# Kernel tuning notes

Hardware: AMD Instinct MI355X
Metric: run time of the kernel (lower is better)

Reference implementation:

```python
import jax, jax.numpy as jnp
import numpy as np

B, M, SV, OV, R, L, V, E = 256, 10, 32, 32, 128, 12, 1000, 64
M2 = M * M
STATE_DIM = (SV + 1) * M2  # 3300
OBJ_DIM = OV * M2          # 3200


def setup_inputs() -> dict:
    key = jax.random.key(0)
    ks = jax.random.split(key, 24)
    s = 0.02
    inp = {
        "state": jax.random.randint(ks[0], (B, M2), 0, SV),
        "obj": jax.random.randint(ks[1], (B, M2), 0, OV),
        "text": jax.random.randint(ks[2], (B, L), 0, V),
        # state MLP [STATE_DIM,128,128,R]
        "Ws1": jax.random.normal(ks[3], (STATE_DIM, 128)) * s,
        "bs1": jnp.zeros((128,)),
        "Ws2": jax.random.normal(ks[4], (128, 128)) * s,
        "bs2": jnp.zeros((128,)),
        "Ws3": jax.random.normal(ks[5], (128, R)) * s,
        "bs3": jnp.zeros((R,)),
        # object MLP [OBJ_DIM,128,128,R]
        "Wo1": jax.random.normal(ks[6], (OBJ_DIM, 128)) * s,
        "bo1": jnp.zeros((128,)),
        "Wo2": jax.random.normal(ks[7], (128, 128)) * s,
        "bo2": jnp.zeros((128,)),
        "Wo3": jax.random.normal(ks[8], (128, R)) * s,
        "bo3": jnp.zeros((R,)),
        # LSTM text encoder: embedding + single-layer LSTM with hidden=R
        "emb": jax.random.normal(ks[9], (V, E)) * s,
        "Wih": jax.random.normal(ks[10], (E, 4 * R)) * s,
        "Whh": jax.random.normal(ks[11], (R, 4 * R)) * s,
        "b_lstm": jnp.zeros((4 * R,)),
    }
    return inp


def _mlp(x, W1, b1, W2, b2, W3, b3):
    h = jax.nn.relu(x @ W1 + b1)
    h = jax.nn.relu(h @ W2 + b2)
    return h @ W3 + b3


def _lstm_last_hidden(text, emb, Wih, Whh, b):
    # text: (B, L) ids -> final hidden (B, R)
    x = emb[text]                      # (B, L, E)
    xs = jnp.swapaxes(x, 0, 1)         # (L, B, E)
    h0 = jnp.zeros((text.shape[0], R), x.dtype)
    c0 = jnp.zeros((text.shape[0], R), x.dtype)

    def step(carry, xt):
        h, c = carry
        g = xt @ Wih + h @ Whh + b     # (B, 4R)
        i, f, gg, o = jnp.split(g, 4, axis=-1)
        c = jax.nn.sigmoid(f) * c + jax.nn.sigmoid(i) * jnp.tanh(gg)
        h = jax.nn.sigmoid(o) * jnp.tanh(c)
        return (h, c), None

    (h, _), _ = jax.lax.scan(step, (h0, c0), xs)
    return h


def reference(state, obj, text, Ws1, bs1, Ws2, bs2, Ws3, bs3,
              Wo1, bo1, Wo2, bo2, Wo3, bo3, emb, Wih, Whh, b_lstm):
    b = state.shape[0]
    # one-hot encodings (torch scatter_ over channel dim)
    state_oh = jax.nn.one_hot(state, SV, dtype=jnp.float32)   # (B, 100, SV)
    obj_oh = jax.nn.one_hot(obj, OV, dtype=jnp.float32)       # (B, 100, OV)

    # repeat each map map_dim^2 times; copy p gets a one-hot of agent position p
    pos = jnp.eye(M2, dtype=jnp.float32)[None, :, :, None]    # (1, 100 copies, 100 cells, 1)
    state_rep = jnp.broadcast_to(state_oh[:, None], (b, M2, M2, SV))
    state_inp = jnp.concatenate(
        [state_rep, jnp.broadcast_to(pos, (b, M2, M2, 1))], axis=-1
    ).reshape(b * M2, STATE_DIM)
    obj_inp = jnp.broadcast_to(obj_oh[:, None], (b, M2, M2, OV)).reshape(b * M2, OBJ_DIM)

    state_out = _mlp(state_inp, Ws1, bs1, Ws2, bs2, Ws3, bs3)   # (B*100, R)
    object_out = _mlp(obj_inp, Wo1, bo1, Wo2, bo2, Wo3, bo3)    # (B*100, R)

    # text is identical across the 100 copies -> encode once, broadcast
    h = _lstm_last_hidden(text, emb, Wih, Whh, b_lstm)          # (B, R)
    lstm_out = jnp.broadcast_to(h[:, None], (b, M2, R)).reshape(b * M2, R)

    values = state_out * object_out * lstm_out                 # (B*100, R)
    map_pred = values.sum(1).reshape(b, M, M)
    return map_pred
```

## Files before the change

### kernel.cpp

```cpp
#include <hip/hip_runtime.h>


#define B_   256
#define M2_  100
#define R_   128
#define L_   12
#define E_   64
#define NT   1024

typedef _Float16 half2v __attribute__((ext_vector_type(2)));
typedef _Float16 f16x8  __attribute__((ext_vector_type(8)));
typedef float    f32x4  __attribute__((ext_vector_type(4)));

__device__ __forceinline__ float sigf(float x) { return 1.f / (1.f + expf(-x)); }

__device__ __forceinline__ uint pk16(float a, float b) {
    half2v h; h.x = (_Float16)a; h.y = (_Float16)b;
    return __builtin_bit_cast(uint, h);
}

__device__ __forceinline__ float fdot2u(uint a, uint b, float c) {
    half2v ha = __builtin_bit_cast(half2v, a);
    half2v hb = __builtin_bit_cast(half2v, b);
#if __has_builtin(__builtin_amdgcn_fdot2)
    return __builtin_amdgcn_fdot2(ha, hb, c, false);
#else
    return c + (float)ha.x * (float)hb.x + (float)ha.y * (float)hb.y;
#endif
}

#define X6(OP) OP(0) OP(1) OP(2) OP(3) OP(4) OP(5)

__global__ __launch_bounds__(NT, 4) void uvfa_kernel(
    const int* __restrict__ state, const int* __restrict__ obj, const int* __restrict__ text,
    const float* __restrict__ Ws1, const float* __restrict__ bs1,
    const float* __restrict__ Ws2, const float* __restrict__ bs2,
    const float* __restrict__ Ws3, const float* __restrict__ bs3,
    const float* __restrict__ Wo1, const float* __restrict__ bo1,
    const float* __restrict__ Wo2, const float* __restrict__ bo2,
    const float* __restrict__ Wo3, const float* __restrict__ bo3,
    const float* __restrict__ emb, const float* __restrict__ Wih,
    const float* __restrict__ Whh, const float* __restrict__ b_lstm,
    float* __restrict__ out)
{
    const int b   = blockIdx.x;
    const int tid = threadIdx.x;

    __shared__ __align__(16) uint  U[14848];
    __shared__ __align__(16) float part[NT];
    __shared__ __align__(16) float hbuf[R_];
    __shared__ __align__(16) uint  hpair[R_ / 2];
    __shared__ __align__(16) float tmp[R_], tmp2[R_], wbuf[R_], ubuf[R_], bsbuf[R_];
    __shared__ int   idx_o[M2_], idx_s[M2_], tids[L_];
    __shared__ float c0s;

    float* xw   = (float*)U;
    float* xemb = (float*)(U + 6144);

    const int lane = tid & 63;
    const int wv   = tid >> 6;
    const int m16  = lane & 15;
    const int kg   = lane >> 4;

    f16x8 af[2][4];
    #pragma unroll
    for (int tt = 0; tt < 2; ++tt) {
        int col = (2 * wv + tt) * 16 + m16;
        #pragma unroll
        for (int s = 0; s < 4; ++s) {
            int kb = s * 32 + kg * 8;
            #pragma unroll
            for (int e = 0; e < 8; ++e)
                af[tt][s][e] = (_Float16)Whh[(kb + e) * 512 + col];
        }
    }

    if (tid < M2_) idx_o[tid] = obj[b * M2_ + tid];
    else if (tid >= 128 && tid < 128 + M2_) idx_s[tid - 128] = state[b * M2_ + tid - 128];
    else if (tid >= 256 && tid < 256 + L_) tids[tid - 256] = text[b * L_ + tid - 256];
    else if (tid >= 384 && tid < 448) hpair[tid - 384] = 0u;
    __syncthreads();
    if (tid < L_ * E_) xemb[tid] = emb[tids[tid >> 6] * E_ + (tid & 63)];
    __syncthreads();

    {
        const int col = tid & 511, th = tid >> 9;
        float bl = b_lstm[col];
        #define DA(i) float a##i = bl;
        X6(DA)
        const float* xe = xemb + (th * 6) * E_;
        #pragma unroll 8
        for (int e = 0; e < E_; ++e) {
            float we = Wih[e * 512 + col];
            #define FA(i) a##i = fmaf(xe[(i) * E_ + e], we, a##i);
            X6(FA)
        }
        #define SA(i) xw[(th * 6 + (i)) * 512 + col] = a##i;
        X6(SA)
    }
    __syncthreads();

    float cst = 0.f;
    for (int t = 0; t < L_; ++t) {
        f16x8 bf[4];
        #pragma unroll
        for (int s = 0; s < 4; ++s) {
            uint4 hb = *(const uint4*)&hpair[s * 16 + kg * 4];
            bf[s] = __builtin_bit_cast(f16x8, hb);
        }
        #pragma unroll
        for (int tt = 0; tt < 2; ++tt) {
            int colb = (2 * wv + tt) * 16 + kg * 4;
            f32x4 acc = *(const f32x4*)&xw[t * 512 + colb];
            #pragma unroll
            for (int s = 0; s < 4; ++s)
                acc = __builtin_amdgcn_mfma_f32_16x16x32_f16(af[tt][s], bf[s], acc, 0, 0, 0);
            if (m16 == 0) {
                part[colb + 0] = acc[0];
                part[colb + 1] = acc[1];
                part[colb + 2] = acc[2];
                part[colb + 3] = acc[3];
            }
        }
        __syncthreads();
        if (tid < R_) {
            float gi = part[tid], gf = part[R_ + tid], gg = part[2 * R_ + tid], go = part[3 * R_ + tid];
            cst = sigf(gf) * cst + sigf(gi) * tanhf(gg);
            float hn = sigf(go) * tanhf(cst);
            hbuf[tid] = hn;
            float hs = __shfl_down(hn, 1, 64);
            if (!(tid & 1)) hpair[tid >> 1] = pk16(hn, hs);
        }
        __syncthreads();
    }

    #pragma unroll
    for (int idx = tid; idx < 64 * 128; idx += NT) {
        int jp = idx >> 7, kk = idx & 127;
        U[idx] = pk16(Ws2[(2 * jp) * R_ + kk], Ws2[(2 * jp + 1) * R_ + kk]);
    }

    const int k = tid & 127, qq = tid >> 7;
    {
        float acc = 0.f;
        int c0i = qq * 13, c1i = c0i + 13 < M2_ ? c0i + 13 : M2_;
        for (int c = c0i; c < c1i; ++c)
            acc += Wo1[(c * 32 + idx_o[c]) * R_ + k];
        part[qq * R_ + k] = acc;
    }
    __syncthreads();
    if (tid < R_) {
        float a = bo1[tid];
        #pragma unroll
        for (int q8 = 0; q8 < 8; ++q8) a += part[q8 * R_ + tid];
        tmp[tid] = fmaxf(a, 0.f);
    }
    __syncthreads();
    {
        float s0 = 0.f, s1 = 0.f, s2 = 0.f, s3 = 0.f;
        int j0 = qq * 16;
        #pragma unroll
        for (int j = 0; j < 16; j += 4) {
            s0 = fmaf(tmp[j0 + j + 0], Wo2[(j0 + j + 0) * R_ + k], s0);
            s1 = fmaf(tmp[j0 + j + 1], Wo2[(j0 + j + 1) * R_ + k], s1);
            s2 = fmaf(tmp[j0 + j + 2], Wo2[(j0 + j + 2) * R_ + k], s2);
            s3 = fmaf(tmp[j0 + j + 3], Wo2[(j0 + j + 3) * R_ + k], s3);
        }
        part[qq * R_ + k] = (s0 + s1) + (s2 + s3);
    }
    __syncthreads();
    if (tid < R_) {
        float a = bo2[tid];
        #pragma unroll
        for (int q8 = 0; q8 < 8; ++q8) a += part[q8 * R_ + tid];
        tmp2[tid] = fmaxf(a, 0.f);
    }
    __syncthreads();
    {
        float s0 = 0.f, s1 = 0.f, s2 = 0.f, s3 = 0.f;
        int j0 = qq * 16;
        #pragma unroll
        for (int j = 0; j < 16; j += 4) {
            s0 = fmaf(tmp2[j0 + j + 0], Wo3[(j0 + j + 0) * R_ + k], s0);
            s1 = fmaf(tmp2[j0 + j + 1], Wo3[(j0 + j + 1) * R_ + k], s1);
            s2 = fmaf(tmp2[j0 + j + 2], Wo3[(j0 + j + 2) * R_ + k], s2);
            s3 = fmaf(tmp2[j0 + j + 3], Wo3[(j0 + j + 3) * R_ + k], s3);
        }
        part[qq * R_ + k] = (s0 + s1) + (s2 + s3);
    }
    __syncthreads();
    if (tid < R_) {
        float a = bo3[tid];
        #pragma unroll
        for (int q8 = 0; q8 < 8; ++q8) a += part[q8 * R_ + tid];
        wbuf[tid] = a * hbuf[tid];
    }
    __syncthreads();

    {
        float s0 = 0.f, s1 = 0.f, s2 = 0.f, s3 = 0.f;
        int j0 = qq * 16;
        const float4* w3 = reinterpret_cast<const float4*>(&Ws3[k * R_ + j0]);
        #pragma unroll
        for (int jj = 0; jj < 4; ++jj) {
            float4 v = w3[jj];
            s0 = fmaf(v.x, wbuf[j0 + jj * 4 + 0], s0);
            s1 = fmaf(v.y, wbuf[j0 + jj * 4 + 1], s1);
            s2 = fmaf(v.z, wbuf[j0 + jj * 4 + 2], s2);
            s3 = fmaf(v.w, wbuf[j0 + jj * 4 + 3], s3);
        }
        part[qq * R_ + k] = (s0 + s1) + (s2 + s3);
    }
    if (tid >= 960) {
        int j = tid - 960;
        float s = bs3[j] * wbuf[j] + bs3[j + 64] * wbuf[j + 64];
        s += __shfl_down(s, 32, 64);
        s += __shfl_down(s, 16, 64);
        s += __shfl_down(s, 8, 64);
        s += __shfl_down(s, 4, 64);
        s += __shfl_down(s, 2, 64);
        s += __shfl_down(s, 1, 64);
        if (j == 0) c0s = s;
    }
    __syncthreads();
    if (tid < R_) {
        float a = 0.f;
        #pragma unroll
        for (int q8 = 0; q8 < 8; ++q8) a += part[q8 * R_ + tid];
        ubuf[tid] = a;
    }
    __syncthreads();

    {
        float acc = 0.f;
        int c0i = qq * 13, c1i = c0i + 13 < M2_ ? c0i + 13 : M2_;
        for (int c = c0i; c < c1i; ++c)
            acc += Ws1[(c * 33 + idx_s[c]) * R_ + k];
        part[qq * R_ + k] = acc;
    }
    __syncthreads();
    if (tid < R_) {
        float a = bs1[tid];
        #pragma unroll
        for (int q8 = 0; q8 < 8; ++q8) a += part[q8 * R_ + tid];
        bsbuf[tid] = a;
    }
    __syncthreads();

    #pragma unroll 4
    for (int pass = 0; pass < 13; ++pass) {
        int idx = pass * NT + tid;
        if (idx < M2_ * R_) {
            int j = idx & 127, p = idx >> 7;
            float v = fmaxf(bsbuf[j] + Ws1[(p * 33 + 32) * R_ + j], 0.f);
            float v2 = __shfl_down(v, 1, 64);
            if (!(j & 1)) U[8192 + (j >> 1) * 104 + p] = pk16(v, v2);
        }
    }
    __syncthreads();

    if (tid < 400) {
        const int pq = tid >> 4, ko = tid & 15;
        const uint* Wsp = U + 8 * ko;
        const uint* Hp  = U + 8192 + 4 * pq;
        float4 uA = *(const float4*)&ubuf[8 * ko];
        float4 uB = *(const float4*)&ubuf[8 * ko + 4];
        float4 bA = *(const float4*)&bs2[8 * ko];
        float4 bB = *(const float4*)&bs2[8 * ko + 4];
        float acc[4][8];
        #pragma unroll
        for (int pi = 0; pi < 4; ++pi)
            #pragma unroll
            for (int r = 0; r < 8; ++r) acc[pi][r] = 0.f;
        #pragma unroll 2
        for (int jp = 0; jp < 64; ++jp) {
            uint4 hq = *(const uint4*)(Hp  + jp * 104);
            uint4 w0 = *(const uint4*)(Wsp + jp * 128);
            uint4 w1 = *(const uint4*)(Wsp + jp * 128 + 4);
            #pragma unroll
            for (int pi = 0; pi < 4; ++pi) {
                uint hh = pi == 0 ? hq.x : pi == 1 ? hq.y : pi == 2 ? hq.z : hq.w;
                acc[pi][0] = fdot2u(hh, w0.x, acc[pi][0]);
                acc[pi][1] = fdot2u(hh, w0.y, acc[pi][1]);
                acc[pi][2] = fdot2u(hh, w0.z, acc[pi][2]);
                acc[pi][3] = fdot2u(hh, w0.w, acc[pi][3]);
                acc[pi][4] = fdot2u(hh, w1.x, acc[pi][4]);
                acc[pi][5] = fdot2u(hh, w1.y, acc[pi][5]);
                acc[pi][6] = fdot2u(hh, w1.z, acc[pi][6]);
                acc[pi][7] = fdot2u(hh, w1.w, acc[pi][7]);
            }
        }
        #pragma unroll
        for (int pi = 0; pi < 4; ++pi) {
            float s = fmaxf(acc[pi][0] + bA.x, 0.f) * uA.x + fmaxf(acc[pi][1] + bA.y, 0.f) * uA.y
                    + fmaxf(acc[pi][2] + bA.z, 0.f) * uA.z + fmaxf(acc[pi][3] + bA.w, 0.f) * uA.w
                    + fmaxf(acc[pi][4] + bB.x, 0.f) * uB.x + fmaxf(acc[pi][5] + bB.y, 0.f) * uB.y
                    + fmaxf(acc[pi][6] + bB.z, 0.f) * uB.z + fmaxf(acc[pi][7] + bB.w, 0.f) * uB.w;
            s += __shfl_xor(s, 1, 64);
            s += __shfl_xor(s, 2, 64);
            s += __shfl_xor(s, 4, 64);
            s += __shfl_xor(s, 8, 64);
            if (ko == 0) out[b * M2_ + 4 * pq + pi] = s + c0s;
        }
    }
}

extern "C" void kernel_launch(void* const* d_in, const int* in_sizes, int n_in,
                              void* d_out, int out_size, void* d_ws, size_t ws_size,
                              hipStream_t stream) {
    const int*   state  = (const int*)d_in[0];
    const int*   obj    = (const int*)d_in[1];
    const int*   text   = (const int*)d_in[2];
    const float* Ws1    = (const float*)d_in[3];
    const float* bs1    = (const float*)d_in[4];
    const float* Ws2    = (const float*)d_in[5];
    const float* bs2    = (const float*)d_in[6];
    const float* Ws3    = (const float*)d_in[7];
    const float* bs3    = (const float*)d_in[8];
    const float* Wo1    = (const float*)d_in[9];
    const float* bo1    = (const float*)d_in[10];
    const float* Wo2    = (const float*)d_in[11];
    const float* bo2    = (const float*)d_in[12];
    const float* Wo3    = (const float*)d_in[13];
    const float* bo3    = (const float*)d_in[14];
    const float* emb    = (const float*)d_in[15];
    const float* Wih    = (const float*)d_in[16];
    const float* Whh    = (const float*)d_in[17];
    const float* b_lstm = (const float*)d_in[18];
    float* out = (float*)d_out;

    hipLaunchKernelGGL(uvfa_kernel, dim3(B_), dim3(NT), 0, stream,
                       state, obj, text, Ws1, bs1, Ws2, bs2, Ws3, bs3,
                       Wo1, bo1, Wo2, bo2, Wo3, bo3, emb, Wih, Whh, b_lstm, out);
}
```

Baseline: 46.76 us.

## Move LSTM input projection and state-MLP layer-2 onto MFMA matrix instructions

Replaces the scalar FMA input projection (xemb @ Wih) with 16x16x32 f16 MFMA tiles, zero-padding the 12 timesteps to 16. Replaces the fdot2-based per-position layer-2 GEMM with MFMA tiles over 14 waves, using padded shared-memory layouts (stride 66 and 132) to limit bank conflicts. The relu and dot-with-u epilogue is then reduced across two N-halves through a new shared buffer. This adds fp16 rounding to the input projection, extra LDS footprint and one more barrier.

Result: faster. 39.34 us (-15.9%).

```diff
diff --git a/kernel.cpp b/kernel.cpp
--- a/kernel.cpp
+++ b/kernel.cpp
@@ -18,18 +18,6 @@
     half2v h; h.x = (_Float16)a; h.y = (_Float16)b;
     return __builtin_bit_cast(uint, h);
 }
-
-__device__ __forceinline__ float fdot2u(uint a, uint b, float c) {
-    half2v ha = __builtin_bit_cast(half2v, a);
-    half2v hb = __builtin_bit_cast(half2v, b);
-#if __has_builtin(__builtin_amdgcn_fdot2)
-    return __builtin_amdgcn_fdot2(ha, hb, c, false);
-#else
-    return c + (float)ha.x * (float)hb.x + (float)ha.y * (float)hb.y;
-#endif
-}
-
-#define X6(OP) OP(0) OP(1) OP(2) OP(3) OP(4) OP(5)
 
 __global__ __launch_bounds__(NT, 4) void uvfa_kernel(
     const int* __restrict__ state, const int* __restrict__ obj, const int* __restrict__ text,
@@ -46,21 +34,22 @@
     const int b   = blockIdx.x;
     const int tid = threadIdx.x;
 
-    __shared__ __align__(16) uint  U[14848];
+    __shared__ __align__(16) uint  U[15840];
     __shared__ __align__(16) float part[NT];
     __shared__ __align__(16) float hbuf[R_];
     __shared__ __align__(16) uint  hpair[R_ / 2];
     __shared__ __align__(16) float tmp[R_], tmp2[R_], wbuf[R_], ubuf[R_], bsbuf[R_];
+    __shared__ float redw2[2][112];
     __shared__ int   idx_o[M2_], idx_s[M2_], tids[L_];
     __shared__ float c0s;
 
     float* xw   = (float*)U;
-    float* xemb = (float*)(U + 6144);
+    float* xemb = (float*)(U + 8192);
 
     const int lane = tid & 63;
     const int wv   = tid >> 6;
     const int m16  = lane & 15;
-    const int kg   = lane >> 4;
+    const int kgrp = lane >> 4;
 
     f16x8 af[2][4];
     #pragma unroll
@@ -68,7 +57,7 @@
         int col = (2 * wv + tt) * 16 + m16;
         #pragma unroll
         for (int s = 0; s < 4; ++s) {
-            int kb = s * 32 + kg * 8;
+            int kb = s * 32 + kgrp * 8;
             #pragma unroll
             for (int e = 0; e < 8; ++e)
                 af[tt][s][e] = (_Float16)Whh[(kb + e) * 512 + col];
@@ -80,23 +69,37 @@
     else if (tid >= 256 && tid < 256 + L_) tids[tid - 256] = text[b * L_ + tid - 256];
     else if (tid >= 384 && tid < 448) hpair[tid - 384] = 0u;
     __syncthreads();
-    if (tid < L_ * E_) xemb[tid] = emb[tids[tid >> 6] * E_ + (tid & 63)];
-    __syncthreads();
-
-    {
-        const int col = tid & 511, th = tid >> 9;
-        float bl = b_lstm[col];
-        #define DA(i) float a##i = bl;
-        X6(DA)
-        const float* xe = xemb + (th * 6) * E_;
-        #pragma unroll 8
-        for (int e = 0; e < E_; ++e) {
-            float we = Wih[e * 512 + col];
-            #define FA(i) a##i = fmaf(xe[(i) * E_ + e], we, a##i);
-            X6(FA)
-        }
-        #define SA(i) xw[(th * 6 + (i)) * 512 + col] = a##i;
-        X6(SA)
+    if (tid < L_ * E_) xemb[(tid >> 6) * 66 + (tid & 63)] = emb[tids[tid >> 6] * E_ + (tid & 63)];
+    else if (tid < L_ * E_ + 264) ((float*)(U + 8192 + 792))[tid - L_ * E_] = 0.f;
+    __syncthreads();
+
+    {
+        f16x8 ax[2];
+        #pragma unroll
+        for (int s = 0; s < 2; ++s) {
+            #pragma unroll
+            for (int e = 0; e < 8; ++e)
+                ax[s][e] = (_Float16)xemb[m16 * 66 + s * 32 + kgrp * 8 + e];
+        }
+        #pragma unroll
+        for (int h = 0; h < 2; ++h) {
+            int col = (wv * 2 + h) * 16 + m16;
+            float bl = b_lstm[col];
+            f32x4 acc = { bl, bl, bl, bl };
+            #pragma unroll
+            for (int s = 0; s < 2; ++s) {
+                f16x8 bx;
+                #pragma unroll
+                for (int e = 0; e < 8; ++e)
+                    bx[e] = (_Float16)Wih[(s * 32 + kgrp * 8 + e) * 512 + col];
+                acc = __builtin_amdgcn_mfma_f32_16x16x32_f16(ax[s], bx, acc, 0, 0, 0);
+            }
+            if (kgrp < 3) {
+                #pragma unroll
+                for (int r = 0; r < 4; ++r)
+                    xw[(kgrp * 4 + r) * 512 + col] = acc[r];
+            }
+        }
     }
     __syncthreads();
 
@@ -105,12 +108,12 @@
         f16x8 bf[4];
         #pragma unroll
         for (int s = 0; s < 4; ++s) {
-            uint4 hb = *(const uint4*)&hpair[s * 16 + kg * 4];
+            uint4 hb = *(const uint4*)&hpair[s * 16 + kgrp * 4];
             bf[s] = __builtin_bit_cast(f16x8, hb);
         }
         #pragma unroll
         for (int tt = 0; tt < 2; ++tt) {
-            int colb = (2 * wv + tt) * 16 + kg * 4;
+            int colb = (2 * wv + tt) * 16 + kgrp * 4;
             f32x4 acc = *(const f32x4*)&xw[t * 512 + colb];
             #pragma unroll
             for (int s = 0; s < 4; ++s)
@@ -137,7 +140,7 @@
     #pragma unroll
     for (int idx = tid; idx < 64 * 128; idx += NT) {
         int jp = idx >> 7, kk = idx & 127;
-        U[idx] = pk16(Ws2[(2 * jp) * R_ + kk], Ws2[(2 * jp + 1) * R_ + kk]);
+        U[jp * 132 + kk] = pk16(Ws2[(2 * jp) * R_ + kk], Ws2[(2 * jp + 1) * R_ + kk]);
     }
 
     const int k = tid & 127, qq = tid >> 7;
@@ -254,55 +257,64 @@
             int j = idx & 127, p = idx >> 7;
             float v = fmaxf(bsbuf[j] + Ws1[(p * 33 + 32) * R_ + j], 0.f);
             float v2 = __shfl_down(v, 1, 64);
-            if (!(j & 1)) U[8192 + (j >> 1) * 104 + p] = pk16(v, v2);
-        }
-    }
-    __syncthreads();
-
-    if (tid < 400) {
-        const int pq = tid >> 4, ko = tid & 15;
-        const uint* Wsp = U + 8 * ko;
-        const uint* Hp  = U + 8192 + 4 * pq;
-        float4 uA = *(const float4*)&ubuf[8 * ko];
-        float4 uB = *(const float4*)&ubuf[8 * ko + 4];
-        float4 bA = *(const float4*)&bs2[8 * ko];
-        float4 bB = *(const float4*)&bs2[8 * ko + 4];
-        float acc[4][8];
-        #pragma unroll
-        for (int pi = 0; pi < 4; ++pi)
-            #pragma unroll
-            for (int r = 0; r < 8; ++r) acc[pi][r] = 0.f;
-        #pragma unroll 2
-        for (int jp = 0; jp < 64; ++jp) {
-            uint4 hq = *(const uint4*)(Hp  + jp * 104);
-            uint4 w0 = *(const uint4*)(Wsp + jp * 128);
-            uint4 w1 = *(const uint4*)(Wsp + jp * 128 + 4);
-            #pragma unroll
-            for (int pi = 0; pi < 4; ++pi) {
-                uint hh = pi == 0 ? hq.x : pi == 1 ? hq.y : pi == 2 ? hq.z : hq.w;
-                acc[pi][0] = fdot2u(hh, w0.x, acc[pi][0]);
-                acc[pi][1] = fdot2u(hh, w0.y, acc[pi][1]);
-                acc[pi][2] = fdot2u(hh, w0.z, acc[pi][2]);
-                acc[pi][3] = fdot2u(hh, w0.w, acc[pi][3]);
-                acc[pi][4] = fdot2u(hh, w1.x, acc[pi][4]);
-                acc[pi][5] = fdot2u(hh, w1.y, acc[pi][5]);
-                acc[pi][6] = fdot2u(hh, w1.z, acc[pi][6]);
-                acc[pi][7] = fdot2u(hh, w1.w, acc[pi][7]);
+            if (!(j & 1)) U[8448 + p * 66 + (j >> 1)] = pk16(v, v2);
+        }
+    }
+    if (tid < 792) U[8448 + 6600 + tid] = 0u;
+    __syncthreads();
+
+    if (wv < 14) {
+        const int mtile = wv >> 1, nhalf = wv & 1;
+        const uint* Ap = U + 8448 + (mtile * 16 + m16) * 66;
+        f16x8 A[4];
+        #pragma unroll
+        for (int s = 0; s < 4; ++s) {
+            int jb = s * 16 + kgrp * 4;
+            uint4 av = { Ap[jb + 0], Ap[jb + 1], Ap[jb + 2], Ap[jb + 3] };
+            A[s] = __builtin_bit_cast(f16x8, av);
+        }
+        f32x4 acc[4] = { {0,0,0,0}, {0,0,0,0}, {0,0,0,0}, {0,0,0,0} };
+        #pragma unroll
+        for (int nt = 0; nt < 4; ++nt) {
+            int ko = (nhalf * 4 + nt) * 16 + m16;
+            #pragma unroll
+            for (int s = 0; s < 4; ++s) {
+                const uint* Bp = U + (s * 16 + kgrp * 4) * 132 + ko;
+                uint4 bv = { Bp[0], Bp[132], Bp[264], Bp[396] };
+                acc[nt] = __builtin_amdgcn_mfma_f32_16x16x32_f16(
+                    A[s], __builtin_bit_cast(f16x8, bv), acc[nt], 0, 0, 0);
             }
         }
-        #pragma unroll
-        for (int pi = 0; pi < 4; ++pi) {
-            float s = fmaxf(acc[pi][0] + bA.x, 0.f) * uA.x + fmaxf(acc[pi][1] + bA.y, 0.f) * uA.y
-                    + fmaxf(acc[pi][2] + bA.z, 0.f) * uA.z + fmaxf(acc[pi][3] + bA.w, 0.f) * uA.w
-                    + fmaxf(acc[pi][4] + bB.x, 0.f) * uB.x + fmaxf(acc[pi][5] + bB.y, 0.f) * uB.y
-                    + fmaxf(acc[pi][6] + bB.z, 0.f) * uB.z + fmaxf(acc[pi][7] + bB.w, 0.f) * uB.w;
-            s += __shfl_xor(s, 1, 64);
-            s += __shfl_xor(s, 2, 64);
-            s += __shfl_xor(s, 4, 64);
-            s += __shfl_xor(s, 8, 64);
-            if (ko == 0) out[b * M2_ + 4 * pq + pi] = s + c0s;
-        }
-    }
+        float vs0 = 0.f, vs1 = 0.f, vs2 = 0.f, vs3 = 0.f;
+        #pragma unroll
+        for (int nt = 0; nt < 4; ++nt) {
+            int ko = (nhalf * 4 + nt) * 16 + m16;
+            float bb = bs2[ko], uu = ubuf[ko];
+            vs0 = fmaf(fmaxf(acc[nt][0] + bb, 0.f), uu, vs0);
+            vs1 = fmaf(fmaxf(acc[nt][1] + bb, 0.f), uu, vs1);
+            vs2 = fmaf(fmaxf(acc[nt][2] + bb, 0.f), uu, vs2);
+            vs3 = fmaf(fmaxf(acc[nt][3] + bb, 0.f), uu, vs3);
+        }
+        vs0 += __shfl_xor(vs0, 1, 64); vs0 += __shfl_xor(vs0, 2, 64);
+        vs0 += __shfl_xor(vs0, 4, 64); vs0 += __shfl_xor(vs0, 8, 64);
+        vs1 += __shfl_xor(vs1, 1, 64); vs1 += __shfl_xor(vs1, 2, 64);
+        vs1 += __shfl_xor(vs1, 4, 64); vs1 += __shfl_xor(vs1, 8, 64);
+        vs2 += __shfl_xor(vs2, 1, 64); vs2 += __shfl_xor(vs2, 2, 64);
+        vs2 += __shfl_xor(vs2, 4, 64); vs2 += __shfl_xor(vs2, 8, 64);
+        vs3 += __shfl_xor(vs3, 1, 64); vs3 += __shfl_xor(vs3, 2, 64);
+        vs3 += __shfl_xor(vs3, 4, 64); vs3 += __shfl_xor(vs3, 8, 64);
+        if (m16 == 0) {
+            int pr = mtile * 16 + kgrp * 4;
+            redw2[nhalf][pr + 0] = vs0;
+            redw2[nhalf][pr + 1] = vs1;
+            redw2[nhalf][pr + 2] = vs2;
+            redw2[nhalf][pr + 3] = vs3;
+        }
+    }
+    __syncthreads();
+
+    if (tid < M2_)
+        out[b * M2_ + tid] = c0s + redw2[0][tid] + redw2[1][tid];
 }
 
 extern "C" void kernel_launch(void* const* d_in, const int* in_sizes, int n_in,
```
